# Optimization experiments

Hardware: AMD Instinct MI355X
Metric: run time of the kernel (lower is better)

## Reference

```python
import jax, jax.numpy as jnp
import numpy as np

N_ITEMS = 6000
D = 64
L = 200
B = 32


def setup_inputs() -> dict:
    key = jax.random.key(0)
    ks = jax.random.split(key, 30)
    g = lambda k, shape: jax.random.normal(k, shape, dtype=jnp.float32) * 0.1
    u = jax.random.uniform(ks[0], (N_ITEMS + 1, N_ITEMS + 1), dtype=jnp.float32)
    adj = jnp.where(u > 0.99, u, 0.0)
    item_emb = g(ks[1], (N_ITEMS + 1, D)).at[0].set(0.0)  # padding_idx=0
    return {
        "log_seqs": jax.random.randint(ks[2], (B, L), 0, N_ITEMS + 1),
        "pos_seqs": jax.random.randint(ks[3], (B, L), 0, N_ITEMS + 1),
        "neg_seqs": jax.random.randint(ks[4], (B, L), 0, N_ITEMS + 1),
        "step": 1,
        "adj": adj,
        "item_emb": item_emb,
        "pos_emb_table": g(ks[5], (L, D)),
        "W_item": g(ks[6], (D, D)),
        "a_item": g(ks[7], (2 * D, 1)),
        "W_1": g(ks[8], (D, D)),
        "W_2": g(ks[9], (D, D)),
        "b_attn": g(ks[10], (D, 1)),
        "co_center": g(ks[11], (D, D)),
        "co_neighbor": g(ks[12], (D, D)),
        "conv1_w": g(ks[13], (D, D)),
        "conv1_b": g(ks[14], (D,)),
        "conv2_w": g(ks[15], (D, D)),
        "conv2_b": g(ks[16], (D,)),
        "up_w": g(ks[17], (D, 2 * D)),
        "up_b": g(ks[18], (2 * D,)),
        "gate_w": g(ks[19], (D, 2 * D)),
        "gate_b": g(ks[20], (2 * D,)),
        "down_w": g(ks[21], (2 * D, D)),
        "down_b": g(ks[22], (D,)),
    }


def reference(log_seqs, pos_seqs, neg_seqs, step, adj, item_emb, pos_emb_table,
              W_item, a_item, W_1, W_2, b_attn, co_center, co_neighbor,
              conv1_w, conv1_b, conv2_w, conv2_b,
              up_w, up_b, gate_w, gate_b, down_w, down_b):
    # ---- update(): GAT over dense item-item adjacency ----
    h_item = item_emb @ W_item                      # [N+1, D]
    wh1 = h_item @ a_item[:D]                       # [N+1, 1]
    wh2 = h_item @ a_item[D:]                       # [N+1, 1]
    e_item = jax.nn.leaky_relu(wh1 + wh2.T)         # [N+1, N+1]
    attn_all = jax.nn.softmax(jnp.where(adj > 0, e_item, -9e15), axis=1)
    trans_info = adj @ h_item                       # [N+1, D]
    gat_info = attn_all @ h_item                    # [N+1, D]

    # ---- log2feats ----
    gat_n = gat_info[log_seqs]                      # [B, L, D]
    trans_n = trans_info[log_seqs]
    seqs_self = item_emb[log_seqs]
    coff = jax.nn.sigmoid(gat_n @ co_center + trans_n @ co_neighbor)
    seqs = coff * gat_n + (1.0 - coff) * trans_n + seqs_self
    # dropout disabled (eval)
    not_pad = (log_seqs != 0)[..., None].astype(seqs.dtype)  # [B, L, 1]
    pos = pos_emb_table[None, :, :] * not_pad
    seqs_pos = seqs + pos

    M1 = seqs_pos @ W_1
    M2 = seqs_pos @ W_2
    # sigmoid(M1_q + M2_k) projected by b -> [B, L, L]
    score = jnp.einsum('bqkd,d->bqk',
                       jax.nn.sigmoid(M1[:, :, None, :] + M2[:, None, :, :]),
                       b_attn[:, 0])
    Lq = seqs_pos.shape[1]
    causal = jnp.tril(jnp.ones((Lq, Lq), dtype=score.dtype))
    score = score * causal                          # masked_fill(mask==0, 0)
    final = jnp.einsum('bqk,bkd->bqd', score, seqs)

    # PointWiseFeedForward (dropout off)
    final = final + (jax.nn.relu(final @ conv1_w + conv1_b) @ conv2_w + conv2_b)
    # UpDown (dropout off)
    y_up = final @ up_w + up_b
    gate = jax.nn.relu(final @ gate_w + gate_b)
    final = final + jax.nn.relu((gate * y_up) @ down_w + down_b)

    pos_logits = jnp.sum(final * item_emb[pos_seqs], axis=-1)  # [B, L]
    neg_logits = jnp.sum(final * item_emb[neg_seqs], axis=-1)  # [B, L]
    return (pos_logits, neg_logits)
```

## Files before the change

### kernel.cpp

```cpp
#include <hip/hip_runtime.h>
#include <hip/hip_bf16.h>
#include <cstddef>

#define NP1 6001
#define BLn 6400
#define TRI 20100

__global__ __launch_bounds__(256) void k_init(int* used) {
    int i = blockIdx.x * 256 + threadIdx.x;
    if (i < NP1) used[i] = 0;
}

__global__ __launch_bounds__(256) void k_mark(const int* logs, int* used) {
    int i = blockIdx.x * 256 + threadIdx.x;
    if (i < BLn) used[logs[i]] = 1;
}

__global__ __launch_bounds__(256) void k_hitem(const float* emb, const float* Wi,
                                               const float* a_item,
                                               float* h, float* wh1, float* wh2) {
    __shared__ float Wl[4096];
    int tid = threadIdx.x;
    {
        const float4* w4 = (const float4*)Wi;
        float4* l4 = (float4*)Wl;
        for (int i = tid; i < 1024; i += 256) l4[i] = w4[i];
    }
    __syncthreads();
    int wave = tid >> 6, lane = tid & 63;
    int row = blockIdx.x * 4 + wave;
    if (row >= NP1) return;
    float e = emb[(size_t)row * 64 + lane];
    float acc = 0.f;
    #pragma unroll
    for (int k = 0; k < 64; k++) acc += __shfl(e, k, 64) * Wl[k * 64 + lane];
    h[(size_t)row * 64 + lane] = acc;
    float p1 = acc * a_item[lane];
    float p2 = acc * a_item[64 + lane];
    for (int off = 32; off > 0; off >>= 1) {
        p1 += __shfl_down(p1, off, 64);
        p2 += __shfl_down(p2, off, 64);
    }
    if (lane == 0) { wh1[row] = p1; wh2[row] = p2; }
}

#define MAXNZ 1024
__global__ __launch_bounds__(256) void k_gat(const float* adj, const float* h,
                                             const float* wh1, const float* wh2,
                                             const int* used, float* gat, float* trans) {
    int row = blockIdx.x;
    if (!used[row]) return;
    __shared__ int s_j[MAXNZ];
    __shared__ float s_a[MAXNZ];
    __shared__ float s_e[MAXNZ];
    __shared__ int s_cnt;
    __shared__ float s_part[4];
    __shared__ float s_g[4][64];
    __shared__ float s_t[4][64];
    int tid = threadIdx.x;
    if (tid == 0) s_cnt = 0;
    __syncthreads();
    float w1 = wh1[row];
    const float* arow = adj + (size_t)row * NP1;
    float ssum = 0.f;

    int j0 = (4 - (row & 3)) & 3;
    int nv = (NP1 - j0) >> 2;

    for (int j = tid; j < j0; j += 256) {
        float a = arow[j];
        if (a > 0.f) {
            float e = w1 + wh2[j];
            e = e > 0.f ? e : 0.01f * e;
            float ee = __expf(e);
            ssum += ee;
            int pos = atomicAdd(&s_cnt, 1);
            if (pos < MAXNZ) { s_j[pos] = j; s_a[pos] = a; s_e[pos] = ee; }
        }
    }
    const float4* av = (const float4*)(arow + j0);
    for (int v = tid; v < nv; v += 256) {
        float4 a4 = av[v];
        int jb = j0 + 4 * v;
        float av4[4] = {a4.x, a4.y, a4.z, a4.w};
        #pragma unroll
        for (int c = 0; c < 4; c++) {
            float a = av4[c];
            if (a > 0.f) {
                int j = jb + c;
                float e = w1 + wh2[j];
                e = e > 0.f ? e : 0.01f * e;
                float ee = __expf(e);
                ssum += ee;
                int pos = atomicAdd(&s_cnt, 1);
                if (pos < MAXNZ) { s_j[pos] = j; s_a[pos] = a; s_e[pos] = ee; }
            }
        }
    }
    for (int j = j0 + 4 * nv + tid; j < NP1; j += 256) {
        float a = arow[j];
        if (a > 0.f) {
            float e = w1 + wh2[j];
            e = e > 0.f ? e : 0.01f * e;
            float ee = __expf(e);
            ssum += ee;
            int pos = atomicAdd(&s_cnt, 1);
            if (pos < MAXNZ) { s_j[pos] = j; s_a[pos] = a; s_e[pos] = ee; }
        }
    }

    int lane = tid & 63, g = tid >> 6;
    for (int o = 32; o > 0; o >>= 1) ssum += __shfl_xor(ssum, o, 64);
    if (lane == 0) s_part[g] = ssum;
    __syncthreads();
    float inv = __builtin_amdgcn_rcpf(s_part[0] + s_part[1] + s_part[2] + s_part[3]);
    int cnt = min(s_cnt, MAXNZ);
    float gacc = 0.f, tacc = 0.f;
    for (int i = g; i < cnt; i += 4) {
        int j = s_j[i];
        float hv = h[(size_t)j * 64 + lane];
        gacc += s_e[i] * hv;
        tacc += s_a[i] * hv;
    }
    s_g[g][lane] = gacc * inv;
    s_t[g][lane] = tacc;
    __syncthreads();
    if (g == 0) {
        gat[(size_t)row * 64 + lane]   = s_g[0][lane] + s_g[1][lane] + s_g[2][lane] + s_g[3][lane];
        trans[(size_t)row * 64 + lane] = s_t[0][lane] + s_t[1][lane] + s_t[2][lane] + s_t[3][lane];
    }
}

__global__ __launch_bounds__(256) void k_seq(const int* logs, const float* gat, const float* trans,
                                             const float* emb, const float* posemb,
                                             const float* cc_, const float* cn_,
                                             const float* W1_, const float* W2_,
                                             float* seqs, float* M1, float* M2T) {
    __shared__ float cc[4096], cn[4096], W1[4096], W2[4096];
    int tid = threadIdx.x;
    {
        float4* c4 = (float4*)cc; float4* n4 = (float4*)cn;
        float4* w14 = (float4*)W1; float4* w24 = (float4*)W2;
        const float4* sc = (const float4*)cc_; const float4* sn = (const float4*)cn_;
        const float4* s1 = (const float4*)W1_; const float4* s2 = (const float4*)W2_;
        for (int i = tid; i < 1024; i += 256) {
            c4[i] = sc[i]; n4[i] = sn[i]; w14[i] = s1[i]; w24[i] = s2[i];
        }
    }
    __syncthreads();
    int wave = tid >> 6, lane = tid & 63;
    for (int i = 0; i < 2; i++) {
        int p = blockIdx.x * 8 + wave * 2 + i;
        int b = p / 200, l = p - b * 200;
        int n = logs[p];
        float g = gat[(size_t)n * 64 + lane];
        float t = trans[(size_t)n * 64 + lane];
        float se = emb[(size_t)n * 64 + lane];
        float ci = 0.f;
        #pragma unroll
        for (int k = 0; k < 64; k++) {
            float gk = __shfl(g, k, 64), tk = __shfl(t, k, 64);
            ci += gk * cc[k * 64 + lane] + tk * cn[k * 64 + lane];
        }
        float coff = 1.f / (1.f + __expf(-ci));
        float s = coff * g + (1.f - coff) * t + se;
        seqs[(size_t)p * 64 + lane] = s;
        float sp = s + (n != 0 ? posemb[l * 64 + lane] : 0.f);
        float m1 = 0.f, m2 = 0.f;
        #pragma unroll
        for (int k = 0; k < 64; k++) {
            float sk = __shfl(sp, k, 64);
            m1 += sk * W1[k * 64 + lane];
            m2 += sk * W2[k * 64 + lane];
        }
        M1[(size_t)p * 64 + lane] = m1;
        M2T[((size_t)b * 64 + lane) * 200 + l] = m2;
    }
}

__global__ __launch_bounds__(256) void k_score(const float* M1, const float* M2T,
                                               const float* battn, float* score) {
    __shared__ float bv[64];
    int tid = threadIdx.x;
    if (tid < 64) bv[tid] = battn[tid];
    __syncthreads();
    int idx = blockIdx.x * 256 + tid;
    if (idx >= TRI * 32) return;
    int b = idx / TRI;
    int t = idx - b * TRI;
    int q = (int)((sqrtf(8.0f * (float)t + 1.0f) - 1.0f) * 0.5f);
    while ((q + 1) * (q + 2) / 2 <= t) q++;
    while (q * (q + 1) / 2 > t) q--;
    int k = t - q * (q + 1) / 2;
    const float* m1 = M1 + ((size_t)(b * 200 + q)) * 64;
    const float* m2 = M2T + (size_t)b * 12800 + k;
    float s = 0.f;
    #pragma unroll 8
    for (int d = 0; d < 64; d++) {
        float x = m1[d] + m2[(size_t)d * 200];
        float e = __expf(-x);
        s += bv[d] * __builtin_amdgcn_rcpf(1.0f + e);
    }
    score[((size_t)(b * 200 + q)) * 200 + k] = s;
}

__global__ __launch_bounds__(256) void k_finffn(const float* score, const float* seqs,
                                                const int* poss, const int* negs,
                                                const float* emb,
                                                const float* c1w, const float* c1b,
                                                const float* c2w, const float* c2b,
                                                const float* upw, const float* upb,
                                                const float* gw, const float* gb,
                                                const float* dw, const float* db,
                                                float* out) {
    __shared__ float wl[16384];
    int tid = threadIdx.x;
    {
        float4* l4 = (float4*)wl;
        const float4* a4 = (const float4*)c1w;
        const float4* b4 = (const float4*)c2w;
        const float4* d4 = (const float4*)dw;
        for (int i = tid; i < 1024; i += 256) l4[i] = a4[i];
        for (int i = tid; i < 1024; i += 256) l4[1024 + i] = b4[i];
        for (int i = tid; i < 2048; i += 256) l4[2048 + i] = d4[i];
    }
    __syncthreads();
    int wave = tid >> 6, lane = tid & 63;
    int p = blockIdx.x * 4 + wave;
    int b = p / 200, q = p - b * 200;

    const float* srow = score + (size_t)p * 200;
    const float* sq = seqs + (size_t)b * 12800;
    float a0 = 0.f, a1 = 0.f, a2 = 0.f, a3 = 0.f;
    int k = 0;
    for (; k + 3 <= q; k += 4) {
        float4 s4 = *(const float4*)(srow + k);
        a0 += s4.x * sq[(k + 0) * 64 + lane];
        a1 += s4.y * sq[(k + 1) * 64 + lane];
        a2 += s4.z * sq[(k + 2) * 64 + lane];
        a3 += s4.w * sq[(k + 3) * 64 + lane];
    }
    for (; k <= q; k++) a0 += srow[k] * sq[k * 64 + lane];
    float x = (a0 + a1) + (a2 + a3);

    float acc = c1b[lane];
    #pragma unroll
    for (int kk = 0; kk < 64; kk++) acc += __shfl(x, kk, 64) * wl[kk * 64 + lane];
    float h1 = acc > 0.f ? acc : 0.f;
    acc = c2b[lane];
    #pragma unroll
    for (int kk = 0; kk < 64; kk++) acc += __shfl(h1, kk, 64) * wl[4096 + kk * 64 + lane];
    float x2 = x + acc;
    float u0 = upb[lane], u1 = upb[64 + lane];
    float g0 = gb[lane],  g1 = gb[64 + lane];
    #pragma unroll
    for (int kk = 0; kk < 64; kk++) {
        float xk = __shfl(x2, kk, 64);
        u0 += xk * upw[kk * 128 + lane];
        u1 += xk * upw[kk * 128 + 64 + lane];
        g0 += xk * gw[kk * 128 + lane];
        g1 += xk * gw[kk * 128 + 64 + lane];
    }
    g0 = g0 > 0.f ? g0 : 0.f;
    g1 = g1 > 0.f ? g1 : 0.f;
    float hh0 = g0 * u0, hh1 = g1 * u1;
    acc = db[lane];
    #pragma unroll
    for (int kk = 0; kk < 64; kk++) acc += __shfl(hh0, kk, 64) * wl[8192 + kk * 64 + lane];
    #pragma unroll
    for (int kk = 0; kk < 64; kk++) acc += __shfl(hh1, kk, 64) * wl[8192 + (64 + kk) * 64 + lane];
    float x3 = x2 + (acc > 0.f ? acc : 0.f);
    int pn = poss[p], nn = negs[p];
    float pl = x3 * emb[(size_t)pn * 64 + lane];
    float nl = x3 * emb[(size_t)nn * 64 + lane];
    for (int o = 32; o > 0; o >>= 1) {
        pl += __shfl_xor(pl, o, 64);
        nl += __shfl_xor(nl, o, 64);
    }
    if (lane == 0) { out[p] = pl; out[BLn + p] = nl; }
}

extern "C" void kernel_launch(void* const* d_in, const int* in_sizes, int n_in,
                              void* d_out, int out_size, void* d_ws, size_t ws_size,
                              hipStream_t stream) {
    const int* logs = (const int*)d_in[0];
    const int* poss = (const int*)d_in[1];
    const int* negs = (const int*)d_in[2];
    const float* adj      = (const float*)d_in[4];
    const float* item_emb = (const float*)d_in[5];
    const float* posemb   = (const float*)d_in[6];
    const float* W_item   = (const float*)d_in[7];
    const float* a_item   = (const float*)d_in[8];
    const float* W_1      = (const float*)d_in[9];
    const float* W_2      = (const float*)d_in[10];
    const float* b_attn   = (const float*)d_in[11];
    const float* cc       = (const float*)d_in[12];
    const float* cn       = (const float*)d_in[13];
    const float* c1w      = (const float*)d_in[14];
    const float* c1b      = (const float*)d_in[15];
    const float* c2w      = (const float*)d_in[16];
    const float* c2b      = (const float*)d_in[17];
    const float* upw      = (const float*)d_in[18];
    const float* upb      = (const float*)d_in[19];
    const float* gw       = (const float*)d_in[20];
    const float* gb       = (const float*)d_in[21];
    const float* dw       = (const float*)d_in[22];
    const float* db       = (const float*)d_in[23];
    float* out = (float*)d_out;

    float* W = (float*)d_ws;
    size_t off = 0;
    float* h_item = W + off; off += 384064;
    float* wh1    = W + off; off += 6016;
    float* wh2    = W + off; off += 6016;
    int*   used   = (int*)(W + off); off += 6016;
    float* gat    = W + off; off += 384064;
    float* trans  = W + off; off += 384064;
    float* seqs   = W + off; off += 409600;
    float* M1     = W + off; off += 409600;
    float* M2T    = W + off; off += 409600;
    float* score  = W + off; off += 1280000;

    k_init  <<<24, 256, 0, stream>>>(used);
    k_mark  <<<25, 256, 0, stream>>>(logs, used);
    k_hitem <<<1501, 256, 0, stream>>>(item_emb, W_item, a_item, h_item, wh1, wh2);
    k_gat   <<<6001, 256, 0, stream>>>(adj, h_item, wh1, wh2, used, gat, trans);
    k_seq   <<<800, 256, 0, stream>>>(logs, gat, trans, item_emb, posemb, cc, cn, W_1, W_2,
                                      seqs, M1, M2T);
    k_score <<<2513, 256, 0, stream>>>(M1, M2T, b_attn, score);
    k_finffn<<<1600, 256, 0, stream>>>(score, seqs, poss, negs, item_emb,
                                       c1w, c1b, c2w, c2b, upw, upb, gw, gb, dw, db, out);
}
```

Before: 420.7 us.

## Fold used-flag init into k_hitem, defer GAT exp pass, split score accumulators

The separate init kernel goes away: k_hitem now zeroes the used flags and runs before k_mark, saving one launch. In k_gat the adjacency scan now only records nonzero indices and values. The leaky-relu and exp work moves to a second compacted pass over the collected entries, so the divergent scan branch is lighter. k_score uses four independent accumulators with full unrolling for more ILP, and the finffn inner loop gets an unroll-2 pragma.

```diff
diff --git a/kernel.cpp b/kernel.cpp
--- a/kernel.cpp
+++ b/kernel.cpp
@@ -6,11 +6,6 @@
 #define BLn 6400
 #define TRI 20100
 
-__global__ __launch_bounds__(256) void k_init(int* used) {
-    int i = blockIdx.x * 256 + threadIdx.x;
-    if (i < NP1) used[i] = 0;
-}
-
 __global__ __launch_bounds__(256) void k_mark(const int* logs, int* used) {
     int i = blockIdx.x * 256 + threadIdx.x;
     if (i < BLn) used[logs[i]] = 1;
@@ -18,9 +13,11 @@
 
 __global__ __launch_bounds__(256) void k_hitem(const float* emb, const float* Wi,
                                                const float* a_item,
-                                               float* h, float* wh1, float* wh2) {
+                                               float* h, float* wh1, float* wh2, int* used) {
     __shared__ float Wl[4096];
     int tid = threadIdx.x;
+    int gid = blockIdx.x * 256 + tid;
+    if (gid < NP1) used[gid] = 0;
     {
         const float4* w4 = (const float4*)Wi;
         float4* l4 = (float4*)Wl;
@@ -60,9 +57,7 @@
     int tid = threadIdx.x;
     if (tid == 0) s_cnt = 0;
     __syncthreads();
-    float w1 = wh1[row];
     const float* arow = adj + (size_t)row * NP1;
-    float ssum = 0.f;
 
     int j0 = (4 - (row & 3)) & 3;
     int nv = (NP1 - j0) >> 2;
@@ -70,51 +65,42 @@
     for (int j = tid; j < j0; j += 256) {
         float a = arow[j];
         if (a > 0.f) {
-            float e = w1 + wh2[j];
-            e = e > 0.f ? e : 0.01f * e;
-            float ee = __expf(e);
-            ssum += ee;
             int pos = atomicAdd(&s_cnt, 1);
-            if (pos < MAXNZ) { s_j[pos] = j; s_a[pos] = a; s_e[pos] = ee; }
+            if (pos < MAXNZ) { s_j[pos] = j; s_a[pos] = a; }
         }
     }
     const float4* av = (const float4*)(arow + j0);
     for (int v = tid; v < nv; v += 256) {
         float4 a4 = av[v];
         int jb = j0 + 4 * v;
-        float av4[4] = {a4.x, a4.y, a4.z, a4.w};
-        #pragma unroll
-        for (int c = 0; c < 4; c++) {
-            float a = av4[c];
-            if (a > 0.f) {
-                int j = jb + c;
-                float e = w1 + wh2[j];
-                e = e > 0.f ? e : 0.01f * e;
-                float ee = __expf(e);
-                ssum += ee;
-                int pos = atomicAdd(&s_cnt, 1);
-                if (pos < MAXNZ) { s_j[pos] = j; s_a[pos] = a; s_e[pos] = ee; }
-            }
-        }
+        if (a4.x > 0.f) { int pos = atomicAdd(&s_cnt, 1); if (pos < MAXNZ) { s_j[pos] = jb;     s_a[pos] = a4.x; } }
+        if (a4.y > 0.f) { int pos = atomicAdd(&s_cnt, 1); if (pos < MAXNZ) { s_j[pos] = jb + 1; s_a[pos] = a4.y; } }
+        if (a4.z > 0.f) { int pos = atomicAdd(&s_cnt, 1); if (pos < MAXNZ) { s_j[pos] = jb + 2; s_a[pos] = a4.z; } }
+        if (a4.w > 0.f) { int pos = atomicAdd(&s_cnt, 1); if (pos < MAXNZ) { s_j[pos] = jb + 3; s_a[pos] = a4.w; } }
     }
     for (int j = j0 + 4 * nv + tid; j < NP1; j += 256) {
         float a = arow[j];
         if (a > 0.f) {
-            float e = w1 + wh2[j];
-            e = e > 0.f ? e : 0.01f * e;
-            float ee = __expf(e);
-            ssum += ee;
             int pos = atomicAdd(&s_cnt, 1);
-            if (pos < MAXNZ) { s_j[pos] = j; s_a[pos] = a; s_e[pos] = ee; }
-        }
-    }
-
+            if (pos < MAXNZ) { s_j[pos] = j; s_a[pos] = a; }
+        }
+    }
+    __syncthreads();
+    int cnt = min(s_cnt, MAXNZ);
+    float w1 = wh1[row];
+    float ssum = 0.f;
+    for (int i = tid; i < cnt; i += 256) {
+        float e = w1 + wh2[s_j[i]];
+        e = e > 0.f ? e : 0.01f * e;
+        float ee = __expf(e);
+        s_e[i] = ee;
+        ssum += ee;
+    }
     int lane = tid & 63, g = tid >> 6;
     for (int o = 32; o > 0; o >>= 1) ssum += __shfl_xor(ssum, o, 64);
     if (lane == 0) s_part[g] = ssum;
     __syncthreads();
     float inv = __builtin_amdgcn_rcpf(s_part[0] + s_part[1] + s_part[2] + s_part[3]);
-    int cnt = min(s_cnt, MAXNZ);
     float gacc = 0.f, tacc = 0.f;
     for (int i = g; i < cnt; i += 4) {
         int j = s_j[i];
@@ -194,14 +180,19 @@
     int k = t - q * (q + 1) / 2;
     const float* m1 = M1 + ((size_t)(b * 200 + q)) * 64;
     const float* m2 = M2T + (size_t)b * 12800 + k;
-    float s = 0.f;
-    #pragma unroll 8
-    for (int d = 0; d < 64; d++) {
-        float x = m1[d] + m2[(size_t)d * 200];
-        float e = __expf(-x);
-        s += bv[d] * __builtin_amdgcn_rcpf(1.0f + e);
-    }
-    score[((size_t)(b * 200 + q)) * 200 + k] = s;
+    float s0 = 0.f, s1 = 0.f, s2 = 0.f, s3 = 0.f;
+    #pragma unroll
+    for (int d = 0; d < 64; d += 4) {
+        float x0 = m1[d + 0] + m2[(size_t)(d + 0) * 200];
+        float x1 = m1[d + 1] + m2[(size_t)(d + 1) * 200];
+        float x2 = m1[d + 2] + m2[(size_t)(d + 2) * 200];
+        float x3 = m1[d + 3] + m2[(size_t)(d + 3) * 200];
+        s0 += bv[d + 0] * __builtin_amdgcn_rcpf(1.0f + __expf(-x0));
+        s1 += bv[d + 1] * __builtin_amdgcn_rcpf(1.0f + __expf(-x1));
+        s2 += bv[d + 2] * __builtin_amdgcn_rcpf(1.0f + __expf(-x2));
+        s3 += bv[d + 3] * __builtin_amdgcn_rcpf(1.0f + __expf(-x3));
+    }
+    score[((size_t)(b * 200 + q)) * 200 + k] = (s0 + s1) + (s2 + s3);
 }
 
 __global__ __launch_bounds__(256) void k_finffn(const float* score, const float* seqs,
@@ -233,6 +224,7 @@
     const float* sq = seqs + (size_t)b * 12800;
     float a0 = 0.f, a1 = 0.f, a2 = 0.f, a3 = 0.f;
     int k = 0;
+    #pragma unroll 2
     for (; k + 3 <= q; k += 4) {
         float4 s4 = *(const float4*)(srow + k);
         a0 += s4.x * sq[(k + 0) * 64 + lane];
@@ -321,9 +313,8 @@
     float* M2T    = W + off; off += 409600;
     float* score  = W + off; off += 1280000;
 
-    k_init  <<<24, 256, 0, stream>>>(used);
+    k_hitem <<<1501, 256, 0, stream>>>(item_emb, W_item, a_item, h_item, wh1, wh2, used);
     k_mark  <<<25, 256, 0, stream>>>(logs, used);
-    k_hitem <<<1501, 256, 0, stream>>>(item_emb, W_item, a_item, h_item, wh1, wh2);
     k_gat   <<<6001, 256, 0, stream>>>(adj, h_item, wh1, wh2, used, gat, trans);
     k_seq   <<<800, 256, 0, stream>>>(logs, gat, trans, item_emb, posemb, cc, cn, W_1, W_2,
                                       seqs, M1, M2T);
```

New measurement: 412.6 us (median of 2 runs). About the same (-1.9%).
